# Kernel optimization log

Measured on AMD Instinct MI355X. Metric: run time of the kernel, lower is better.

The kernel has to match this reference:

```python
import jax, jax.numpy as jnp
import numpy as np

HEAD_SIZE = 64


def setup_inputs() -> dict:
    key = jax.random.key(0)
    ks = jax.random.split(key, 8)
    B, S, W, H = 16, 2048, 768, HEAD_SIZE
    inp = jax.random.normal(ks[0], (B, S, W), dtype=jnp.float32)
    # key-padding mask, broadcastable to [B, S, S]; ensure at least one valid key per row
    mask = jax.random.randint(ks[1], (B, 1, S), 0, 2, dtype=jnp.int32)
    mask = mask.at[:, :, 0].set(1)
    scale = 1.0 / np.sqrt(W)
    Wq = jax.random.normal(ks[2], (W, H), dtype=jnp.float32) * scale
    bq = jax.random.normal(ks[3], (H,), dtype=jnp.float32) * 0.02
    Wk = jax.random.normal(ks[4], (W, H), dtype=jnp.float32) * scale
    bk = jax.random.normal(ks[5], (H,), dtype=jnp.float32) * 0.02
    Wv = jax.random.normal(ks[6], (W, H), dtype=jnp.float32) * scale
    bv = jax.random.normal(ks[7], (H,), dtype=jnp.float32) * 0.02
    return {"input": inp, "mask": mask, "Wq": Wq, "bq": bq, "Wk": Wk, "bk": bk, "Wv": Wv, "bv": bv}


def reference(input, mask, Wq, bq, Wk, bk, Wv, bv):
    # Q/K/V projections: [B, S, H]
    Q = input @ Wq + bq
    K = input @ Wk + bk
    V = input @ Wv + bv
    # scores: [B, S, S], scaled by sqrt(head_size)
    scores = jnp.einsum("bqh,bkh->bqk", Q, K) / jnp.sqrt(jnp.float32(HEAD_SIZE))
    scores = jnp.where(mask == 0, -jnp.inf, scores)
    attn = jax.nn.softmax(scores, axis=-1)
    return jnp.einsum("bqk,bkh->bqh", attn, V)
```

## Files before the change

kernel.cpp:

```cpp
#include <hip/hip_runtime.h>

typedef short bf16x8 __attribute__((ext_vector_type(8)));
typedef float f32x4 __attribute__((ext_vector_type(4)));
typedef float f32x16 __attribute__((ext_vector_type(16)));
typedef unsigned int u32x4 __attribute__((ext_vector_type(4)));
typedef unsigned short u16;
typedef unsigned int u32;

#define DEVI static __device__ __forceinline__

#define NB 16
#define NS 2048
#define NW 768
#define NH 64

DEVI u16 f2bf(float x) {
  u32 u = __builtin_bit_cast(u32, x);
  u += 0x7fffu + ((u >> 16) & 1u);
  return (u16)(u >> 16);
}

DEVI u32 cvtpk(float lo, float hi) {
  u32 r;
  asm("v_cvt_pk_bf16_f32 %0, %1, %2" : "=v"(r) : "v"(lo), "v"(hi));
  return r;
}

DEVI f32x4 mfma16(bf16x8 a, bf16x8 b, f32x4 c) {
  return __builtin_amdgcn_mfma_f32_16x16x32_bf16(a, b, c, 0, 0, 0);
}
DEVI f32x16 mfma32(bf16x8 a, bf16x8 b, f32x16 c) {
  return __builtin_amdgcn_mfma_f32_32x32x16_bf16(a, b, c, 0, 0, 0);
}

DEVI int swz(int row, int col) { return ((row * 64 + col) * 2) ^ ((row & 7) << 4); }


__global__ __launch_bounds__(256) void prep_weights(
    const float* __restrict__ Wq, const float* __restrict__ Wk,
    const float* __restrict__ Wv, u16* __restrict__ wsW) {
  int tid = blockIdx.x * 256 + threadIdx.x;
  int tile = tid >> 6, lane = tid & 63;
  int p = tile / 96, rem = tile % 96;
  int nct = rem / 24, kch = rem % 24;
  const float* Wsrc = (p == 0) ? Wq : ((p == 1) ? Wk : Wv);
  int k0 = kch * 32 + (lane >> 4) * 8;
  int n = nct * 16 + (lane & 15);
  u16 h[8];
#pragma unroll
  for (int i = 0; i < 8; i++) h[i] = f2bf(Wsrc[(k0 + i) * NH + n]);
  uint4 v;
  v.x = (u32)h[0] | ((u32)h[1] << 16);
  v.y = (u32)h[2] | ((u32)h[3] << 16);
  v.z = (u32)h[4] | ((u32)h[5] << 16);
  v.w = (u32)h[6] | ((u32)h[7] << 16);
  ((uint4*)wsW)[tile * 64 + lane] = v;
}

__global__ __launch_bounds__(512, 4) void qkv_proj(
    const float* __restrict__ inp, const u16* __restrict__ wsW,
    const float* __restrict__ bq, const float* __restrict__ bk,
    const float* __restrict__ bv, u16* __restrict__ Qf, u16* __restrict__ Kf,
    u16* __restrict__ Vf) {
  __shared__ __align__(16) u16 A_lds[2][64 * 64];
  int tid = threadIdx.x;
  int w = tid >> 6, lane = tid & 63, g = lane >> 4, l15 = lane & 15;
  int wr = w >> 2, wc = w & 3;
  int row0 = blockIdx.x * 64;
  int sr0 = tid >> 4, sc4 = (tid & 15) * 4, sr1 = sr0 + 32;
  const float* base = inp + (size_t)row0 * NW;

  f32x4 acc[2][3];
#pragma unroll
  for (int rt = 0; rt < 2; rt++)
#pragma unroll
    for (int ct = 0; ct < 3; ct++) acc[rt][ct] = (f32x4)0.0f;

  float4 a0, a1;
  bf16x8 wreg[3][2], wnxt[3][2];

  a0 = *(const float4*)(base + (size_t)sr0 * NW + sc4);
  a1 = *(const float4*)(base + (size_t)sr1 * NW + sc4);
#pragma unroll
  for (int ct = 0; ct < 3; ct++)
#pragma unroll
    for (int kk = 0; kk < 2; kk++)
      wreg[ct][kk] = *(const bf16x8*)(
          wsW + (size_t)((wc * 3 + ct) * 24 + kk) * 512 + lane * 8);
  {
    ushort4 h4;
    h4.x = f2bf(a0.x); h4.y = f2bf(a0.y); h4.z = f2bf(a0.z); h4.w = f2bf(a0.w);
    *(ushort4*)((char*)A_lds[0] + swz(sr0, sc4)) = h4;
    h4.x = f2bf(a1.x); h4.y = f2bf(a1.y); h4.z = f2bf(a1.z); h4.w = f2bf(a1.w);
    *(ushort4*)((char*)A_lds[0] + swz(sr1, sc4)) = h4;
  }
  a0 = *(const float4*)(base + (size_t)sr0 * NW + 64 + sc4);
  a1 = *(const float4*)(base + (size_t)sr1 * NW + 64 + sc4);
#pragma unroll
  for (int ct = 0; ct < 3; ct++)
#pragma unroll
    for (int kk = 0; kk < 2; kk++)
      wnxt[ct][kk] = *(const bf16x8*)(
          wsW + (size_t)((wc * 3 + ct) * 24 + 2 + kk) * 512 + lane * 8);
  __syncthreads();

  int cur = 0;
  for (int t = 0; t < 12; t++) {
    if (t < 11) {
      ushort4 h4;
      h4.x = f2bf(a0.x); h4.y = f2bf(a0.y); h4.z = f2bf(a0.z); h4.w = f2bf(a0.w);
      *(ushort4*)((char*)A_lds[cur ^ 1] + swz(sr0, sc4)) = h4;
      h4.x = f2bf(a1.x); h4.y = f2bf(a1.y); h4.z = f2bf(a1.z); h4.w = f2bf(a1.w);
      *(ushort4*)((char*)A_lds[cur ^ 1] + swz(sr1, sc4)) = h4;
      int c2 = (t < 10) ? t + 2 : 11;
      a0 = *(const float4*)(base + (size_t)sr0 * NW + c2 * 64 + sc4);
      a1 = *(const float4*)(base + (size_t)sr1 * NW + c2 * 64 + sc4);
    }
    bf16x8 af[2][2];
#pragma unroll
    for (int rt = 0; rt < 2; rt++)
#pragma unroll
      for (int kk = 0; kk < 2; kk++)
        af[rt][kk] = *(const bf16x8*)((const char*)A_lds[cur] +
                                      swz(wr * 32 + rt * 16 + l15,
                                          kk * 32 + g * 8));
#pragma unroll
    for (int ct = 0; ct < 3; ct++)
#pragma unroll
      for (int kk = 0; kk < 2; kk++) {
        acc[0][ct] = mfma16(af[0][kk], wreg[ct][kk], acc[0][ct]);
        acc[1][ct] = mfma16(af[1][kk], wreg[ct][kk], acc[1][ct]);
      }
    if (t < 11) {
      int c2 = (t < 10) ? t + 2 : 11;
#pragma unroll
      for (int ct = 0; ct < 3; ct++)
#pragma unroll
        for (int kk = 0; kk < 2; kk++) {
          wreg[ct][kk] = wnxt[ct][kk];
          wnxt[ct][kk] = *(const bf16x8*)(
              wsW + (size_t)((wc * 3 + ct) * 24 + c2 * 2 + kk) * 512 + lane * 8);
        }
    }
    __syncthreads();
    cur ^= 1;
  }

  int b = row0 >> 11;
  size_t bT = (size_t)b * 64 + ((row0 & 2047) >> 5) + wr;
#pragma unroll
  for (int ct = 0; ct < 3; ct++) {
    int gct = wc * 3 + ct;
    int p3 = gct >> 2;
    int n = (gct & 3) * 16 + l15;
    const float* bias = (p3 == 0) ? bq : ((p3 == 1) ? bk : bv);
    float bbv = bias[n];
    if (p3 < 2) {
      u16* basep = (p3 == 0) ? Qf : Kf;
      int kk = gct & 3;
      int hin = (l15 >> 3) & 1, j = l15 & 7;
#pragma unroll
      for (int rt = 0; rt < 2; rt++)
#pragma unroll
        for (int reg = 0; reg < 4; reg++)
          basep[((bT * 4 + kk) * 64 + hin * 32 + rt * 16 + g * 4 + reg) * 8 + j] =
              f2bf(acc[rt][ct][reg] + bbv);
    } else {
      int ht = n >> 5, lanev = ((g >> 1) & 1) * 32 + (n & 31), jb = (g & 1) * 4;
#pragma unroll
      for (int rt = 0; rt < 2; rt++) {
        uint2 pp;
        pp.x = (u32)f2bf(acc[rt][ct][0] + bbv) |
               ((u32)f2bf(acc[rt][ct][1] + bbv) << 16);
        pp.y = (u32)f2bf(acc[rt][ct][2] + bbv) |
               ((u32)f2bf(acc[rt][ct][3] + bbv) << 16);
        *(uint2*)(Vf + (((bT * 2 + rt) * 2 + ht) * 64 + lanev) * 8 + jb) = pp;
      }
    }
  }
}

__global__ __launch_bounds__(512) void attn(
    const u16* __restrict__ Qf, const u16* __restrict__ Kf,
    const u16* __restrict__ Vf, const int* __restrict__ mask,
    float* __restrict__ out) {
  __shared__ __align__(16) char smem[68608];
  int tid = threadIdx.x;
  int w = tid >> 6, lane = tid & 63;
  int l31 = lane & 31, hi = lane >> 5;
  int qt = w >> 2, kc = w & 3;
  int bid = blockIdx.x;
  int b = (bid & 7) * 2 + ((bid >> 3) & 1);
  int qp = bid >> 4;
  const int* mb = mask + (size_t)b * NS;
  float* corrL = (float*)smem + w * 32;

  const float SC = 0.18033688011112043f;

  size_t bQT = (size_t)b * 64 + qp * 2 + qt;
  bf16x8 qf[4];
#pragma unroll
  for (int kk = 0; kk < 4; kk++)
    qf[kk] = *(const bf16x8*)(Qf + (bQT * 4 + kk) * 512 + lane * 8);

  f32x16 acc[2];
  acc[0] = (f32x16)0.0f;
  acc[1] = (f32x16)0.0f;
  float m_run = -1.0e4f, l_run = 0.0f;

  size_t tbase = (size_t)b * 64 + kc * 16;
  bf16x8 kf[4];
#pragma unroll
  for (int kk = 0; kk < 4; kk++)
    kf[kk] = *(const bf16x8*)(Kf + (tbase * 4 + kk) * 512 + lane * 8);

  for (int t = 0; t < 16; t++) {
    int kv0 = kc * 512 + t * 32;
    size_t bKT = tbase + t;
    size_t bKN = tbase + ((t < 15) ? t + 1 : t);
    bf16x8 kn[4];
#pragma unroll
    for (int kk = 0; kk < 4; kk++)
      kn[kk] = *(const bf16x8*)(Kf + (bKN * 4 + kk) * 512 + lane * 8);
    bf16x8 vf[2][2];
#pragma unroll
    for (int ht = 0; ht < 2; ht++)
#pragma unroll
      for (int ks = 0; ks < 2; ks++)
        vf[ht][ks] = *(const bf16x8*)(Vf + ((bKT * 2 + ks) * 2 + ht) * 512 +
                                      lane * 8);
    int mqa[16];
#pragma unroll
    for (int m = 0; m < 4; m++) {
      int4 v = *(const int4*)(mb + kv0 + m * 8 + hi * 4);
      mqa[m * 4 + 0] = v.x;
      mqa[m * 4 + 1] = v.y;
      mqa[m * 4 + 2] = v.z;
      mqa[m * 4 + 3] = v.w;
    }

    f32x16 sT = (f32x16)0.0f;
    __builtin_amdgcn_s_setprio(1);
#pragma unroll
    for (int kk = 0; kk < 4; kk++) sT = mfma32(kf[kk], qf[kk], sT);
    __builtin_amdgcn_s_setprio(0);

#pragma unroll
    for (int r = 0; r < 16; r++) sT[r] = mqa[r] ? sT[r] * SC : -1.0e5f;
    float tm0 = fmaxf(fmaxf(sT[0], sT[1]), fmaxf(sT[2], sT[3]));
    float tm1 = fmaxf(fmaxf(sT[4], sT[5]), fmaxf(sT[6], sT[7]));
    float tm2 = fmaxf(fmaxf(sT[8], sT[9]), fmaxf(sT[10], sT[11]));
    float tm3 = fmaxf(fmaxf(sT[12], sT[13]), fmaxf(sT[14], sT[15]));
    float tm = fmaxf(fmaxf(tm0, tm1), fmaxf(tm2, tm3));
    tm = fmaxf(tm, __shfl_xor(tm, 32));

    if (!__all(tm <= m_run + 8.0f)) {
      float mn = fmaxf(m_run, tm);
      float corr = exp2f(m_run - mn);
      m_run = mn;
      l_run *= corr;
      if (hi == 0) corrL[l31] = corr;
      float4 c4[4];
#pragma unroll
      for (int m = 0; m < 4; m++)
        c4[m] = *(const float4*)(corrL + m * 8 + hi * 4);
#pragma unroll
      for (int r = 0; r < 16; r++) {
        float cq = c4[r >> 2][r & 3];
        acc[0][r] *= cq;
        acc[1][r] *= cq;
      }
    }

    float p[16];
#pragma unroll
    for (int r = 0; r < 16; r++) p[r] = exp2f(sT[r] - m_run);
    float rs0 = (p[0] + p[1]) + (p[2] + p[3]);
    float rs1 = (p[4] + p[5]) + (p[6] + p[7]);
    float rs2 = (p[8] + p[9]) + (p[10] + p[11]);
    float rs3 = (p[12] + p[13]) + (p[14] + p[15]);
    float rs = (rs0 + rs1) + (rs2 + rs3);
    rs += __shfl_xor(rs, 32);
    l_run += rs;

    u32 c[8];
#pragma unroll
    for (int i = 0; i < 8; i++) c[i] = cvtpk(p[2 * i], p[2 * i + 1]);
    asm volatile("v_permlane32_swap_b32 %0, %1" : "+v"(c[0]), "+v"(c[2]));
    asm volatile("v_permlane32_swap_b32 %0, %1" : "+v"(c[1]), "+v"(c[3]));
    asm volatile("v_permlane32_swap_b32 %0, %1" : "+v"(c[4]), "+v"(c[6]));
    asm volatile("v_permlane32_swap_b32 %0, %1" : "+v"(c[5]), "+v"(c[7]));
    u32x4 w0, w1;
    w0.x = c[0]; w0.y = c[1]; w0.z = c[2]; w0.w = c[3];
    w1.x = c[4]; w1.y = c[5]; w1.z = c[6]; w1.w = c[7];
    bf16x8 pa0 = __builtin_bit_cast(bf16x8, w0);
    bf16x8 pa1 = __builtin_bit_cast(bf16x8, w1);

    __builtin_amdgcn_s_setprio(1);
    acc[0] = mfma32(pa0, vf[0][0], acc[0]);
    acc[1] = mfma32(pa0, vf[1][0], acc[1]);
    acc[0] = mfma32(pa1, vf[0][1], acc[0]);
    acc[1] = mfma32(pa1, vf[1][1], acc[1]);
    __builtin_amdgcn_s_setprio(0);

#pragma unroll
    for (int kk = 0; kk < 4; kk++) kf[kk] = kn[kk];
  }

  __syncthreads();
  float* accL = (float*)smem;
  float* mlL = (float*)(smem + 66560);
#pragma unroll
  for (int ht = 0; ht < 2; ht++)
#pragma unroll
    for (int r = 0; r < 16; r++) {
      int q = (r & 3) + 8 * (r >> 2) + 4 * hi;
      accL[(kc * 64 + qt * 32 + q) * 65 + ht * 32 + l31] = acc[ht][r];
    }
  if (hi == 0) {
    mlL[(kc * 64 + qt * 32 + l31) * 2 + 0] = m_run;
    mlL[(kc * 64 + qt * 32 + l31) * 2 + 1] = l_run;
  }
  __syncthreads();

#pragma unroll
  for (int i = 0; i < 8; i++) {
    int idx = tid + i * 512;
    int row = idx >> 6, h = idx & 63;
    float m[4], l[4];
#pragma unroll
    for (int z = 0; z < 4; z++) {
      m[z] = mlL[(z * 64 + row) * 2 + 0];
      l[z] = mlL[(z * 64 + row) * 2 + 1];
    }
    float M = fmaxf(fmaxf(m[0], m[1]), fmaxf(m[2], m[3]));
    float den = 0.0f, o = 0.0f;
#pragma unroll
    for (int z = 0; z < 4; z++) {
      float e = exp2f(m[z] - M);
      den += e * l[z];
      o += e * accL[(z * 64 + row) * 65 + h];
    }
    out[((size_t)b * NS + qp * 64 + row) * NH + h] = o / den;
  }
}

extern "C" void kernel_launch(void* const* d_in, const int* in_sizes, int n_in,
                              void* d_out, int out_size, void* d_ws,
                              size_t ws_size, hipStream_t stream) {
  const float* inp = (const float*)d_in[0];
  const int* mask = (const int*)d_in[1];
  const float* Wq = (const float*)d_in[2];
  const float* bq = (const float*)d_in[3];
  const float* Wk = (const float*)d_in[4];
  const float* bk = (const float*)d_in[5];
  const float* Wv = (const float*)d_in[6];
  const float* bv = (const float*)d_in[7];
  float* out = (float*)d_out;

  char* ws = (char*)d_ws;
  u16* wsW = (u16*)ws;
  u16* wsQf = (u16*)(ws + (1u << 20));
  u16* wsKf = (u16*)(ws + (1u << 20) + (4u << 20));
  u16* wsVf = (u16*)(ws + (1u << 20) + (8u << 20));

  prep_weights<<<dim3(72), dim3(256), 0, stream>>>(Wq, Wk, Wv, wsW);
  qkv_proj<<<dim3((NB * NS) / 64), dim3(512), 0, stream>>>(inp, wsW, bq, bk,
                                                           bv, wsQf, wsKf, wsVf);
  attn<<<dim3(NB * NS / 64), dim3(512), 0, stream>>>(wsQf, wsKf, wsVf, mask,
                                                     out);
}
```

Measured before the change: 78.06 us.

## Stage full 32-row input slab in LDS once, drop per-chunk double buffering

The QKV projection now uses 256-thread blocks over 32 rows. Each block loads the whole 32x768 input slab, converts it to bf16 with packed cvt instructions and writes it to a swizzled 48KB LDS buffer in one pass. The 12 k-step loop then runs with no barriers. This removes the per-iteration __syncthreads and the double-buffer handoff, and gives more blocks with fewer waves each. The cost is higher LDS use per block, which limits occupancy, and no overlap between global loads and MFMA work inside a block.

```diff
diff --git a/kernel.cpp b/kernel.cpp
--- a/kernel.cpp
+++ b/kernel.cpp
@@ -32,8 +32,6 @@
 DEVI f32x16 mfma32(bf16x8 a, bf16x8 b, f32x16 c) {
   return __builtin_amdgcn_mfma_f32_32x32x16_bf16(a, b, c, 0, 0, 0);
 }
-
-DEVI int swz(int row, int col) { return ((row * 64 + col) * 2) ^ ((row & 7) << 4); }
 
 
 __global__ __launch_bounds__(256) void prep_weights(
@@ -57,73 +55,64 @@
   ((uint4*)wsW)[tile * 64 + lane] = v;
 }
 
-__global__ __launch_bounds__(512, 4) void qkv_proj(
+__global__ __launch_bounds__(256) void qkv_proj(
     const float* __restrict__ inp, const u16* __restrict__ wsW,
     const float* __restrict__ bq, const float* __restrict__ bk,
     const float* __restrict__ bv, u16* __restrict__ Qf, u16* __restrict__ Kf,
     u16* __restrict__ Vf) {
-  __shared__ __align__(16) u16 A_lds[2][64 * 64];
+  __shared__ __align__(16) u16 A_lds[32 * NW];
   int tid = threadIdx.x;
   int w = tid >> 6, lane = tid & 63, g = lane >> 4, l15 = lane & 15;
-  int wr = w >> 2, wc = w & 3;
-  int row0 = blockIdx.x * 64;
-  int sr0 = tid >> 4, sc4 = (tid & 15) * 4, sr1 = sr0 + 32;
+  int row0 = blockIdx.x * 32;
   const float* base = inp + (size_t)row0 * NW;
 
+  bf16x8 wreg[3][2], wnxt[3][2];
+#pragma unroll
+  for (int ct = 0; ct < 3; ct++)
+#pragma unroll
+    for (int kk = 0; kk < 2; kk++) {
+      wreg[ct][kk] = *(const bf16x8*)(
+          wsW + (size_t)((w * 3 + ct) * 24 + kk) * 512 + lane * 8);
+      wnxt[ct][kk] = *(const bf16x8*)(
+          wsW + (size_t)((w * 3 + ct) * 24 + 2 + kk) * 512 + lane * 8);
+    }
+
+#pragma unroll
+  for (int p = 0; p < 12; p++) {
+    int idx = tid + p * 256;
+    int r = idx / 96;
+    int c8 = (idx - r * 96) * 8;
+    const float* src = base + (size_t)r * NW + c8;
+    float4 lo = *(const float4*)src;
+    float4 hi2 = *(const float4*)(src + 4);
+    u32x4 pk;
+    pk.x = cvtpk(lo.x, lo.y);
+    pk.y = cvtpk(lo.z, lo.w);
+    pk.z = cvtpk(hi2.x, hi2.y);
+    pk.w = cvtpk(hi2.z, hi2.w);
+    *(u32x4*)((char*)A_lds + ((r * 1536 + c8 * 2) ^ ((r & 7) << 4))) = pk;
+  }
+  __syncthreads();
+
   f32x4 acc[2][3];
 #pragma unroll
   for (int rt = 0; rt < 2; rt++)
 #pragma unroll
     for (int ct = 0; ct < 3; ct++) acc[rt][ct] = (f32x4)0.0f;
 
-  float4 a0, a1;
-  bf16x8 wreg[3][2], wnxt[3][2];
-
-  a0 = *(const float4*)(base + (size_t)sr0 * NW + sc4);
-  a1 = *(const float4*)(base + (size_t)sr1 * NW + sc4);
-#pragma unroll
-  for (int ct = 0; ct < 3; ct++)
-#pragma unroll
-    for (int kk = 0; kk < 2; kk++)
-      wreg[ct][kk] = *(const bf16x8*)(
-          wsW + (size_t)((wc * 3 + ct) * 24 + kk) * 512 + lane * 8);
-  {
-    ushort4 h4;
-    h4.x = f2bf(a0.x); h4.y = f2bf(a0.y); h4.z = f2bf(a0.z); h4.w = f2bf(a0.w);
-    *(ushort4*)((char*)A_lds[0] + swz(sr0, sc4)) = h4;
-    h4.x = f2bf(a1.x); h4.y = f2bf(a1.y); h4.z = f2bf(a1.z); h4.w = f2bf(a1.w);
-    *(ushort4*)((char*)A_lds[0] + swz(sr1, sc4)) = h4;
-  }
-  a0 = *(const float4*)(base + (size_t)sr0 * NW + 64 + sc4);
-  a1 = *(const float4*)(base + (size_t)sr1 * NW + 64 + sc4);
-#pragma unroll
-  for (int ct = 0; ct < 3; ct++)
-#pragma unroll
-    for (int kk = 0; kk < 2; kk++)
-      wnxt[ct][kk] = *(const bf16x8*)(
-          wsW + (size_t)((wc * 3 + ct) * 24 + 2 + kk) * 512 + lane * 8);
-  __syncthreads();
-
-  int cur = 0;
+  int xorv = (l15 & 7) << 4;
+  int rb0 = (0 * 16 + l15) * 1536 + g * 16;
+  int rb1 = (1 * 16 + l15) * 1536 + g * 16;
+
   for (int t = 0; t < 12; t++) {
-    if (t < 11) {
-      ushort4 h4;
-      h4.x = f2bf(a0.x); h4.y = f2bf(a0.y); h4.z = f2bf(a0.z); h4.w = f2bf(a0.w);
-      *(ushort4*)((char*)A_lds[cur ^ 1] + swz(sr0, sc4)) = h4;
-      h4.x = f2bf(a1.x); h4.y = f2bf(a1.y); h4.z = f2bf(a1.z); h4.w = f2bf(a1.w);
-      *(ushort4*)((char*)A_lds[cur ^ 1] + swz(sr1, sc4)) = h4;
-      int c2 = (t < 10) ? t + 2 : 11;
-      a0 = *(const float4*)(base + (size_t)sr0 * NW + c2 * 64 + sc4);
-      a1 = *(const float4*)(base + (size_t)sr1 * NW + c2 * 64 + sc4);
-    }
     bf16x8 af[2][2];
 #pragma unroll
-    for (int rt = 0; rt < 2; rt++)
-#pragma unroll
-      for (int kk = 0; kk < 2; kk++)
-        af[rt][kk] = *(const bf16x8*)((const char*)A_lds[cur] +
-                                      swz(wr * 32 + rt * 16 + l15,
-                                          kk * 32 + g * 8));
+    for (int kk = 0; kk < 2; kk++) {
+      af[0][kk] = *(const bf16x8*)((const char*)A_lds +
+                                   ((rb0 + t * 128 + kk * 64) ^ xorv));
+      af[1][kk] = *(const bf16x8*)((const char*)A_lds +
+                                   ((rb1 + t * 128 + kk * 64) ^ xorv));
+    }
 #pragma unroll
     for (int ct = 0; ct < 3; ct++)
 #pragma unroll
@@ -139,18 +128,16 @@
         for (int kk = 0; kk < 2; kk++) {
           wreg[ct][kk] = wnxt[ct][kk];
           wnxt[ct][kk] = *(const bf16x8*)(
-              wsW + (size_t)((wc * 3 + ct) * 24 + c2 * 2 + kk) * 512 + lane * 8);
+              wsW + (size_t)((w * 3 + ct) * 24 + c2 * 2 + kk) * 512 + lane * 8);
         }
     }
-    __syncthreads();
-    cur ^= 1;
   }
 
   int b = row0 >> 11;
-  size_t bT = (size_t)b * 64 + ((row0 & 2047) >> 5) + wr;
+  size_t bT = (size_t)b * 64 + ((row0 & 2047) >> 5);
 #pragma unroll
   for (int ct = 0; ct < 3; ct++) {
-    int gct = wc * 3 + ct;
+    int gct = w * 3 + ct;
     int p3 = gct >> 2;
     int n = (gct & 3) * 16 + l15;
     const float* bias = (p3 == 0) ? bq : ((p3 == 1) ? bk : bv);
@@ -365,7 +352,7 @@
   u16* wsVf = (u16*)(ws + (1u << 20) + (8u << 20));
 
   prep_weights<<<dim3(72), dim3(256), 0, stream>>>(Wq, Wk, Wv, wsW);
-  qkv_proj<<<dim3((NB * NS) / 64), dim3(512), 0, stream>>>(inp, wsW, bq, bk,
+  qkv_proj<<<dim3((NB * NS) / 32), dim3(256), 0, stream>>>(inp, wsW, bq, bk,
                                                            bv, wsQf, wsKf, wsVf);
   attn<<<dim3(NB * NS / 64), dim3(512), 0, stream>>>(wsQf, wsKf, wsVf, mask,
                                                      out);
```

After: 81.01 us. 3.8% more time.

## Enlarge QKV projection tile to 128 rows and stage weights in LDS

Applied to the files above, without the earlier changes.

The QKV projection block now covers 128 rows instead of 64, with 8 waves arranged 4x2 so each wave computes 32 rows by 96 columns. Weights are loaded cooperatively into LDS per K-chunk rather than each wave holding them in registers, so weight traffic from global memory is shared across twice as many rows. The double-buffered LDS scheme is replaced by a single buffer with register prefetch and two barriers per chunk, and the occupancy hint in launch_bounds is dropped. This may expose more load latency and halves the grid size, and the larger accumulator set raises register pressure.

```diff
diff --git a/kernel.cpp b/kernel.cpp
--- a/kernel.cpp
+++ b/kernel.cpp
@@ -57,100 +57,96 @@
   ((uint4*)wsW)[tile * 64 + lane] = v;
 }
 
-__global__ __launch_bounds__(512, 4) void qkv_proj(
+__global__ __launch_bounds__(512) void qkv_proj(
     const float* __restrict__ inp, const u16* __restrict__ wsW,
     const float* __restrict__ bq, const float* __restrict__ bk,
     const float* __restrict__ bv, u16* __restrict__ Qf, u16* __restrict__ Kf,
     u16* __restrict__ Vf) {
-  __shared__ __align__(16) u16 A_lds[2][64 * 64];
+  __shared__ __align__(16) u16 A_lds[128 * 64];
+  __shared__ __align__(16) u16 W_lds[24 * 512];
   int tid = threadIdx.x;
   int w = tid >> 6, lane = tid & 63, g = lane >> 4, l15 = lane & 15;
-  int wr = w >> 2, wc = w & 3;
-  int row0 = blockIdx.x * 64;
-  int sr0 = tid >> 4, sc4 = (tid & 15) * 4, sr1 = sr0 + 32;
-  const float* base = inp + (size_t)row0 * NW;
-
-  f32x4 acc[2][3];
+  int wr = w & 3, wc = w >> 2;
+  int row0 = blockIdx.x * 128;
+
+  f32x4 acc[2][6];
 #pragma unroll
   for (int rt = 0; rt < 2; rt++)
 #pragma unroll
-    for (int ct = 0; ct < 3; ct++) acc[rt][ct] = (f32x4)0.0f;
-
-  float4 a0, a1;
-  bf16x8 wreg[3][2], wnxt[3][2];
-
-  a0 = *(const float4*)(base + (size_t)sr0 * NW + sc4);
-  a1 = *(const float4*)(base + (size_t)sr1 * NW + sc4);
-#pragma unroll
-  for (int ct = 0; ct < 3; ct++)
-#pragma unroll
-    for (int kk = 0; kk < 2; kk++)
-      wreg[ct][kk] = *(const bf16x8*)(
-          wsW + (size_t)((wc * 3 + ct) * 24 + kk) * 512 + lane * 8);
-  {
-    ushort4 h4;
-    h4.x = f2bf(a0.x); h4.y = f2bf(a0.y); h4.z = f2bf(a0.z); h4.w = f2bf(a0.w);
-    *(ushort4*)((char*)A_lds[0] + swz(sr0, sc4)) = h4;
-    h4.x = f2bf(a1.x); h4.y = f2bf(a1.y); h4.z = f2bf(a1.z); h4.w = f2bf(a1.w);
-    *(ushort4*)((char*)A_lds[0] + swz(sr1, sc4)) = h4;
-  }
-  a0 = *(const float4*)(base + (size_t)sr0 * NW + 64 + sc4);
-  a1 = *(const float4*)(base + (size_t)sr1 * NW + 64 + sc4);
-#pragma unroll
-  for (int ct = 0; ct < 3; ct++)
-#pragma unroll
-    for (int kk = 0; kk < 2; kk++)
-      wnxt[ct][kk] = *(const bf16x8*)(
-          wsW + (size_t)((wc * 3 + ct) * 24 + 2 + kk) * 512 + lane * 8);
-  __syncthreads();
-
-  int cur = 0;
-  for (int t = 0; t < 12; t++) {
-    if (t < 11) {
+    for (int ct = 0; ct < 6; ct++) acc[rt][ct] = (f32x4)0.0f;
+
+  float4 a_reg[4];
+  uint4 w_reg[3];
+#pragma unroll
+  for (int p = 0; p < 4; p++) {
+    int id = tid + p * 512;
+    int r = id >> 4, c4 = (id & 15) * 4;
+    a_reg[p] = *(const float4*)(inp + (size_t)(row0 + r) * NW + c4);
+  }
+#pragma unroll
+  for (int p = 0; p < 3; p++) {
+    int id = tid + p * 512;
+    int t = id >> 6, ls = id & 63;
+    w_reg[p] = ((const uint4*)wsW)[((t >> 1) * 24 + (t & 1)) * 64 + ls];
+  }
+
+  for (int chunk = 0; chunk < 12; chunk++) {
+    __syncthreads();
+#pragma unroll
+    for (int p = 0; p < 4; p++) {
+      int id = tid + p * 512;
+      int r = id >> 4, c4 = (id & 15) * 4;
+      float4 v = a_reg[p];
       ushort4 h4;
-      h4.x = f2bf(a0.x); h4.y = f2bf(a0.y); h4.z = f2bf(a0.z); h4.w = f2bf(a0.w);
-      *(ushort4*)((char*)A_lds[cur ^ 1] + swz(sr0, sc4)) = h4;
-      h4.x = f2bf(a1.x); h4.y = f2bf(a1.y); h4.z = f2bf(a1.z); h4.w = f2bf(a1.w);
-      *(ushort4*)((char*)A_lds[cur ^ 1] + swz(sr1, sc4)) = h4;
-      int c2 = (t < 10) ? t + 2 : 11;
-      a0 = *(const float4*)(base + (size_t)sr0 * NW + c2 * 64 + sc4);
-      a1 = *(const float4*)(base + (size_t)sr1 * NW + c2 * 64 + sc4);
-    }
+      h4.x = f2bf(v.x); h4.y = f2bf(v.y); h4.z = f2bf(v.z); h4.w = f2bf(v.w);
+      *(ushort4*)((char*)A_lds + swz(r, c4)) = h4;
+    }
+#pragma unroll
+    for (int p = 0; p < 3; p++) {
+      int id = tid + p * 512;
+      int t = id >> 6, ls = id & 63;
+      ((uint4*)W_lds)[t * 64 + ls] = w_reg[p];
+    }
+    if (chunk < 11) {
+      int k0 = (chunk + 1) * 64;
+#pragma unroll
+      for (int p = 0; p < 4; p++) {
+        int id = tid + p * 512;
+        int r = id >> 4, c4 = (id & 15) * 4;
+        a_reg[p] = *(const float4*)(inp + (size_t)(row0 + r) * NW + k0 + c4);
+      }
+#pragma unroll
+      for (int p = 0; p < 3; p++) {
+        int id = tid + p * 512;
+        int t = id >> 6, ls = id & 63;
+        w_reg[p] = ((const uint4*)
+                        wsW)[((t >> 1) * 24 + (chunk + 1) * 2 + (t & 1)) * 64 + ls];
+      }
+    }
+    __syncthreads();
     bf16x8 af[2][2];
 #pragma unroll
     for (int rt = 0; rt < 2; rt++)
 #pragma unroll
       for (int kk = 0; kk < 2; kk++)
-        af[rt][kk] = *(const bf16x8*)((const char*)A_lds[cur] +
-                                      swz(wr * 32 + rt * 16 + l15,
-                                          kk * 32 + g * 8));
-#pragma unroll
-    for (int ct = 0; ct < 3; ct++)
+        af[rt][kk] = *(const bf16x8*)((const char*)A_lds +
+                                      swz(wr * 32 + rt * 16 + l15, kk * 32 + g * 8));
+#pragma unroll
+    for (int ct = 0; ct < 6; ct++)
 #pragma unroll
       for (int kk = 0; kk < 2; kk++) {
-        acc[0][ct] = mfma16(af[0][kk], wreg[ct][kk], acc[0][ct]);
-        acc[1][ct] = mfma16(af[1][kk], wreg[ct][kk], acc[1][ct]);
-      }
-    if (t < 11) {
-      int c2 = (t < 10) ? t + 2 : 11;
-#pragma unroll
-      for (int ct = 0; ct < 3; ct++)
-#pragma unroll
-        for (int kk = 0; kk < 2; kk++) {
-          wreg[ct][kk] = wnxt[ct][kk];
-          wnxt[ct][kk] = *(const bf16x8*)(
-              wsW + (size_t)((wc * 3 + ct) * 24 + c2 * 2 + kk) * 512 + lane * 8);
-        }
-    }
-    __syncthreads();
-    cur ^= 1;
+        bf16x8 bfr = *(const bf16x8*)(W_lds +
+                                      (((wc * 6 + ct) * 2 + kk) * 512 + lane * 8));
+        acc[0][ct] = mfma16(af[0][kk], bfr, acc[0][ct]);
+        acc[1][ct] = mfma16(af[1][kk], bfr, acc[1][ct]);
+      }
   }
 
   int b = row0 >> 11;
   size_t bT = (size_t)b * 64 + ((row0 & 2047) >> 5) + wr;
 #pragma unroll
-  for (int ct = 0; ct < 3; ct++) {
-    int gct = wc * 3 + ct;
+  for (int ct = 0; ct < 6; ct++) {
+    int gct = wc * 6 + ct;
     int p3 = gct >> 2;
     int n = (gct & 3) * 16 + l15;
     const float* bias = (p3 == 0) ? bq : ((p3 == 1) ? bk : bv);
@@ -365,8 +361,9 @@
   u16* wsVf = (u16*)(ws + (1u << 20) + (8u << 20));
 
   prep_weights<<<dim3(72), dim3(256), 0, stream>>>(Wq, Wk, Wv, wsW);
-  qkv_proj<<<dim3((NB * NS) / 64), dim3(512), 0, stream>>>(inp, wsW, bq, bk,
-                                                           bv, wsQf, wsKf, wsVf);
+  qkv_proj<<<dim3((NB * NS) / 128), dim3(512), 0, stream>>>(inp, wsW, bq, bk,
+                                                            bv, wsQf, wsKf,
+                                                            wsVf);
   attn<<<dim3(NB * NS / 64), dim3(512), 0, stream>>>(wsQf, wsKf, wsVf, mask,
                                                      out);
 }
```

Result: slower. 100.3 us (+28.5%).
